# Optimization experiments

Hardware: AMD Instinct MI355X
Metric: run time of the kernel (lower is better)

Reference implementation:

```python
import jax, jax.numpy as jnp
import numpy as np

# Irreps spec: 256x0e + 128x1o + 64x2e + 32x3o (irreps_out == irreps_in)
MULS = (256, 128, 64, 32)          # multiplicities per irrep block
IRDIMS = (1, 3, 5, 7)              # 2l+1 per irrep block
FEAT_DIM = sum(m * d for m, d in zip(MULS, IRDIMS))   # 1184
W_DIM = sum(m * m for m in MULS)                       # 87040
BATCH = 131072


def setup_inputs() -> dict:
    key = jax.random.key(0)
    kx, kw = jax.random.split(key)
    x = jax.random.normal(kx, (BATCH, FEAT_DIM), dtype=jnp.float32)
    w = jax.random.normal(kw, (W_DIM,), dtype=jnp.float32)
    return {"x": x, "w": w}


def reference(x, w):
    """Equivariant linear: per-irrep block-diagonal matmul with 1/sqrt(mul_in) norm.

    x: [B, FEAT_DIM] in mul_ir layout (segments of [mul, 2l+1] flattened).
    w: [W_DIM] flat weights, segments of [mul_out, mul_in] flattened.
    """
    B = x.shape[0]
    outs = []
    xo = 0  # feature offset (static)
    wo = 0  # weight offset (static)
    for mul, d in zip(MULS, IRDIMS):
        seg = x[:, xo:xo + mul * d].reshape(B, mul, d)          # [B, u, i]
        wb = w[wo:wo + mul * mul].reshape(mul, mul)             # [v, u]
        c = 1.0 / np.sqrt(mul)                                  # path normalization
        y = jnp.einsum('vu,bui->bvi', wb * c, seg,
                       precision=jax.lax.Precision.HIGH)        # [B, v, i]
        outs.append(y.reshape(B, mul * d))
        xo += mul * d
        wo += mul * mul
    return jnp.concatenate(outs, axis=-1)  # [B, FEAT_DIM]
```

## Files before the change

kernel.cpp:

```cpp
#include <hip/hip_runtime.h>


typedef __attribute__((ext_vector_type(8))) __bf16 bf16x8;
typedef __attribute__((ext_vector_type(4))) float f32x4;

constexpr int FEAT = 1184;

template<int MUL, int D, int XO, int WO, int WAVES_M, int WAVES_N, int NT>
__global__ __launch_bounds__(256, 2)
void eqlin(const float* __restrict__ x, const float* __restrict__ w,
           float* __restrict__ out, int n_tiles, float cnorm)
{
    constexpr int KS   = MUL / 32;
    constexpr int ROWS = WAVES_M * 16;

    const int tid  = threadIdx.x;
    const int lane = tid & 63;
    const int wid  = tid >> 6;
    const int wm   = wid % WAVES_M;
    const int wn   = wid / WAVES_M;
    const int l16  = lane & 15;
    const int quad = lane >> 4;
    const int lk8  = quad * 8;

    bf16x8 bfrag[NT][KS];
#pragma unroll
    for (int nt = 0; nt < NT; ++nt) {
        const int v = (wn * NT + nt) * 16 + l16;
        const float* wp = w + WO + (long)v * MUL;
#pragma unroll
        for (int ks = 0; ks < KS; ++ks) {
            const int u0 = ks * 32 + lk8;
#pragma unroll
            for (int j = 0; j < 8; ++j)
                bfrag[nt][ks][j] = (__bf16)(wp[u0 + j] * cnorm);
        }
    }

    for (int t = blockIdx.x; t < n_tiles; t += gridDim.x) {
        if (WAVES_N > 1) __syncthreads();

        const int mbase = t * ROWS + wm * 16;

        bf16x8 afrag[KS];
        {
            const int m = mbase + l16;
            if (D == 1) {
                const float* xp = x + (long)m * FEAT + XO;
#pragma unroll
                for (int ks = 0; ks < KS; ++ks) {
                    const float4 p0 = *(const float4*)(xp + ks * 32 + lk8);
                    const float4 p1 = *(const float4*)(xp + ks * 32 + lk8 + 4);
                    afrag[ks][0] = (__bf16)p0.x; afrag[ks][1] = (__bf16)p0.y;
                    afrag[ks][2] = (__bf16)p0.z; afrag[ks][3] = (__bf16)p0.w;
                    afrag[ks][4] = (__bf16)p1.x; afrag[ks][5] = (__bf16)p1.y;
                    afrag[ks][6] = (__bf16)p1.z; afrag[ks][7] = (__bf16)p1.w;
                }
            } else {
                const int b = m / D;
                const int i = m - b * D;
                const float* xp = x + (long)b * FEAT + XO + i;
#pragma unroll
                for (int ks = 0; ks < KS; ++ks) {
#pragma unroll
                    for (int j = 0; j < 8; ++j)
                        afrag[ks][j] = (__bf16)xp[(ks * 32 + lk8 + j) * D];
                }
            }
        }

        f32x4 acc[NT];
#pragma unroll
        for (int nt = 0; nt < NT; ++nt) acc[nt] = f32x4{0.f, 0.f, 0.f, 0.f};
#pragma unroll
        for (int ks = 0; ks < KS; ++ks)
#pragma unroll
            for (int nt = 0; nt < NT; ++nt)
                acc[nt] = __builtin_amdgcn_mfma_f32_16x16x32_bf16(
                    afrag[ks], bfrag[nt][ks], acc[nt], 0, 0, 0);

#pragma unroll
        for (int nt = 0; nt < NT; ++nt) {
            const int v = (wn * NT + nt) * 16 + l16;
#pragma unroll
            for (int r = 0; r < 4; ++r) {
                const int mm = mbase + quad * 4 + r;
                const int b = mm / D;
                const int i = mm - b * D;
                out[(long)b * FEAT + XO + v * D + i] = acc[nt][r];
            }
        }
    }
}

extern "C" void kernel_launch(void* const* d_in, const int* in_sizes, int n_in,
                              void* d_out, int out_size, void* d_ws, size_t ws_size,
                              hipStream_t stream) {
    const float* x = (const float*)d_in[0];
    const float* w = (const float*)d_in[1];
    float* out = (float*)d_out;

    eqlin<256, 1, 0, 0, 1, 4, 4>
        <<<dim3(512), dim3(256), 0, stream>>>(x, w, out, 8192, 0.0625f);
    eqlin<128, 3, 256, 65536, 2, 2, 4>
        <<<dim3(1024), dim3(256), 0, stream>>>(x, w, out, 12288, 0.088388347648318447f);
    eqlin<64, 5, 640, 81920, 4, 1, 4>
        <<<dim3(2048), dim3(256), 0, stream>>>(x, w, out, 10240, 0.125f);
    eqlin<32, 7, 960, 86016, 4, 1, 2>
        <<<dim3(2048), dim3(256), 0, stream>>>(x, w, out, 14336, 0.17677669529663689f);
}
```

Measured before the change: 1.247 ms.

## Stage x tiles through LDS with coalesced loads and double-buffered prefetch

Each block now loads a contiguous tile of batch rows with coalesced float4 reads and converts them to bf16. For d>1 it transposes them into a padded shared-memory buffer, so the old strided per-element gathers go away. A register prefetch of the next tile overlaps the global loads with the MFMA work, and waves are remapped across v-tiles and m-tiles. Output stores for D==1 are reoriented, and tile sizes, grid sizes and occupancy hints are retuned. In exchange the kernel uses more LDS, takes an extra barrier per tile, and may hit bank conflicts on the scalar transposed LDS writes.

Result: faster. 1.135 ms (-9.0%).

```diff
diff --git a/kernel.cpp b/kernel.cpp
--- a/kernel.cpp
+++ b/kernel.cpp
@@ -2,94 +2,168 @@
 
 
 typedef __attribute__((ext_vector_type(8))) __bf16 bf16x8;
+typedef __attribute__((ext_vector_type(4))) __bf16 bf16x4;
 typedef __attribute__((ext_vector_type(4))) float f32x4;
 
 constexpr int FEAT = 1184;
 
-template<int MUL, int D, int XO, int WO, int WAVES_M, int WAVES_N, int NT>
-__global__ __launch_bounds__(256, 2)
+template<int MUL, int D, int XO, int WO, int BT, int MINW>
+__global__ __launch_bounds__(256, MINW)
 void eqlin(const float* __restrict__ x, const float* __restrict__ w,
            float* __restrict__ out, int n_tiles, float cnorm)
 {
     constexpr int KS   = MUL / 32;
-    constexpr int ROWS = WAVES_M * 16;
+    constexpr int SEG  = MUL * D;
+    constexpr int VT   = MUL / 16;
+    constexpr int VTW  = (VT >= 4) ? VT / 4 : 1;
+    constexpr int MT   = BT * D / 16;
+    constexpr int MSP  = (VT >= 4) ? 1 : 4 / VT;
+    constexpr int MTW  = MT / MSP;
+    constexpr int Kp   = MUL + 8;
+    constexpr int BUFE = BT * D * Kp;
+    constexpr int NLD  = BT * SEG / 1024;
+
+    __shared__ __align__(16) __bf16 smem[2 * BUFE];
 
     const int tid  = threadIdx.x;
     const int lane = tid & 63;
     const int wid  = tid >> 6;
-    const int wm   = wid % WAVES_M;
-    const int wn   = wid / WAVES_M;
     const int l16  = lane & 15;
     const int quad = lane >> 4;
-    const int lk8  = quad * 8;
 
-    bf16x8 bfrag[NT][KS];
+    const int vt0 = (VT >= 4) ? wid * VTW : (wid & (VT - 1));
+    const int mt0 = (VT >= 4) ? 0 : (wid / VT) * MTW;
+
+    bf16x8 wfrag[VTW][KS];
 #pragma unroll
-    for (int nt = 0; nt < NT; ++nt) {
-        const int v = (wn * NT + nt) * 16 + l16;
-        const float* wp = w + WO + (long)v * MUL;
+    for (int vt = 0; vt < VTW; ++vt) {
+        const float* wp = w + WO + (long)((vt0 + vt) * 16 + l16) * MUL;
 #pragma unroll
         for (int ks = 0; ks < KS; ++ks) {
-            const int u0 = ks * 32 + lk8;
-#pragma unroll
-            for (int j = 0; j < 8; ++j)
-                bfrag[nt][ks][j] = (__bf16)(wp[u0 + j] * cnorm);
+            const float4 q0 = *(const float4*)(wp + ks * 32 + quad * 8);
+            const float4 q1 = *(const float4*)(wp + ks * 32 + quad * 8 + 4);
+            wfrag[vt][ks][0] = (__bf16)(q0.x * cnorm);
+            wfrag[vt][ks][1] = (__bf16)(q0.y * cnorm);
+            wfrag[vt][ks][2] = (__bf16)(q0.z * cnorm);
+            wfrag[vt][ks][3] = (__bf16)(q0.w * cnorm);
+            wfrag[vt][ks][4] = (__bf16)(q1.x * cnorm);
+            wfrag[vt][ks][5] = (__bf16)(q1.y * cnorm);
+            wfrag[vt][ks][6] = (__bf16)(q1.z * cnorm);
+            wfrag[vt][ks][7] = (__bf16)(q1.w * cnorm);
         }
     }
 
-    for (int t = blockIdx.x; t < n_tiles; t += gridDim.x) {
-        if (WAVES_N > 1) __syncthreads();
+    int xoff[NLD];
+#pragma unroll
+    for (int c = 0; c < NLD; ++c) {
+        const int e  = (c * 256 + tid) * 4;
+        const int bl = e / SEG;
+        xoff[c] = bl * FEAT + XO + (e - bl * SEG);
+    }
 
-        const int mbase = t * ROWS + wm * 16;
+    float4 pf[NLD];
 
-        bf16x8 afrag[KS];
-        {
-            const int m = mbase + l16;
-            if (D == 1) {
-                const float* xp = x + (long)m * FEAT + XO;
+    auto stage_load = [&](int tt) {
+        const float* xb = x + (long)tt * BT * FEAT;
 #pragma unroll
-                for (int ks = 0; ks < KS; ++ks) {
-                    const float4 p0 = *(const float4*)(xp + ks * 32 + lk8);
-                    const float4 p1 = *(const float4*)(xp + ks * 32 + lk8 + 4);
-                    afrag[ks][0] = (__bf16)p0.x; afrag[ks][1] = (__bf16)p0.y;
-                    afrag[ks][2] = (__bf16)p0.z; afrag[ks][3] = (__bf16)p0.w;
-                    afrag[ks][4] = (__bf16)p1.x; afrag[ks][5] = (__bf16)p1.y;
-                    afrag[ks][6] = (__bf16)p1.z; afrag[ks][7] = (__bf16)p1.w;
-                }
+        for (int c = 0; c < NLD; ++c)
+            pf[c] = *(const float4*)(xb + xoff[c]);
+    };
+
+    auto stage_write = [&](int hb) {
+        __bf16* dst = smem + hb * BUFE;
+#pragma unroll
+        for (int c = 0; c < NLD; ++c) {
+            const int e  = (c * 256 + tid) * 4;
+            const int bl = e / SEG;
+            const int fo = e - bl * SEG;
+            if constexpr (D == 1) {
+                bf16x4 v4;
+                v4[0] = (__bf16)pf[c].x; v4[1] = (__bf16)pf[c].y;
+                v4[2] = (__bf16)pf[c].z; v4[3] = (__bf16)pf[c].w;
+                *(bf16x4*)(dst + bl * Kp + fo) = v4;
             } else {
-                const int b = m / D;
-                const int i = m - b * D;
-                const float* xp = x + (long)b * FEAT + XO + i;
+                const float fv[4] = {pf[c].x, pf[c].y, pf[c].z, pf[c].w};
 #pragma unroll
-                for (int ks = 0; ks < KS; ++ks) {
-#pragma unroll
-                    for (int j = 0; j < 8; ++j)
-                        afrag[ks][j] = (__bf16)xp[(ks * 32 + lk8 + j) * D];
+                for (int j = 0; j < 4; ++j) {
+                    const int f = fo + j;
+                    const int u = f / D;
+                    const int i = f - u * D;
+                    dst[(bl * D + i) * Kp + u] = (__bf16)fv[j];
                 }
             }
         }
+    };
 
-        f32x4 acc[NT];
+    const int G = gridDim.x;
+    int t = blockIdx.x;
+
+    if (t < n_tiles) { stage_load(t); stage_write(0); }
+    __syncthreads();
+
+    int buf = 0;
+    for (; t < n_tiles; t += G) {
+        const int tn = t + G;
+        if (tn < n_tiles) stage_load(tn);
+
+        const __bf16* src = smem + buf * BUFE;
+        f32x4 acc[VTW][MTW];
 #pragma unroll
-        for (int nt = 0; nt < NT; ++nt) acc[nt] = f32x4{0.f, 0.f, 0.f, 0.f};
+        for (int vt = 0; vt < VTW; ++vt)
 #pragma unroll
-        for (int ks = 0; ks < KS; ++ks)
-#pragma unroll
-            for (int nt = 0; nt < NT; ++nt)
-                acc[nt] = __builtin_amdgcn_mfma_f32_16x16x32_bf16(
-                    afrag[ks], bfrag[nt][ks], acc[nt], 0, 0, 0);
+            for (int mt = 0; mt < MTW; ++mt)
+                acc[vt][mt] = f32x4{0.f, 0.f, 0.f, 0.f};
 
 #pragma unroll
-        for (int nt = 0; nt < NT; ++nt) {
-            const int v = (wn * NT + nt) * 16 + l16;
+        for (int mt = 0; mt < MTW; ++mt) {
+            const int m = (mt0 + mt) * 16 + l16;
+            bf16x8 xf[KS];
 #pragma unroll
-            for (int r = 0; r < 4; ++r) {
-                const int mm = mbase + quad * 4 + r;
-                const int b = mm / D;
-                const int i = mm - b * D;
-                out[(long)b * FEAT + XO + v * D + i] = acc[nt][r];
-            }
+            for (int ks = 0; ks < KS; ++ks)
+                xf[ks] = *(const bf16x8*)(src + m * Kp + ks * 32 + quad * 8);
+#pragma unroll
+            for (int ks = 0; ks < KS; ++ks)
+#pragma unroll
+                for (int vt = 0; vt < VTW; ++vt) {
+                    if constexpr (D == 1)
+                        acc[vt][mt] = __builtin_amdgcn_mfma_f32_16x16x32_bf16(
+                            xf[ks], wfrag[vt][ks], acc[vt][mt], 0, 0, 0);
+                    else
+                        acc[vt][mt] = __builtin_amdgcn_mfma_f32_16x16x32_bf16(
+                            wfrag[vt][ks], xf[ks], acc[vt][mt], 0, 0, 0);
+                }
         }
+
+        {
+            const long rb = (long)t * BT;
+#pragma unroll
+            for (int vt = 0; vt < VTW; ++vt)
+#pragma unroll
+                for (int mt = 0; mt < MTW; ++mt) {
+                    if constexpr (D == 1) {
+                        const int v = (vt0 + vt) * 16 + l16;
+#pragma unroll
+                        for (int r = 0; r < 4; ++r) {
+                            const long b = rb + (mt0 + mt) * 16 + quad * 4 + r;
+                            out[b * FEAT + XO + v] = acc[vt][mt][r];
+                        }
+                    } else {
+                        const int m  = (mt0 + mt) * 16 + l16;
+                        const int bl = m / D;
+                        const int i  = m - bl * D;
+#pragma unroll
+                        for (int r = 0; r < 4; ++r) {
+                            const int v = (vt0 + vt) * 16 + quad * 4 + r;
+                            out[(rb + bl) * FEAT + XO + v * D + i] =
+                                acc[vt][mt][r];
+                        }
+                    }
+                }
+        }
+
+        if (tn < n_tiles) stage_write(buf ^ 1);
+        __syncthreads();
+        buf ^= 1;
     }
 }
 
@@ -100,12 +174,12 @@
     const float* w = (const float*)d_in[1];
     float* out = (float*)d_out;
 
-    eqlin<256, 1, 0, 0, 1, 4, 4>
+    eqlin<256, 1,   0,     0, 16, 2>
         <<<dim3(512), dim3(256), 0, stream>>>(x, w, out, 8192, 0.0625f);
-    eqlin<128, 3, 256, 65536, 2, 2, 4>
-        <<<dim3(1024), dim3(256), 0, stream>>>(x, w, out, 12288, 0.088388347648318447f);
-    eqlin<64, 5, 640, 81920, 4, 1, 4>
-        <<<dim3(2048), dim3(256), 0, stream>>>(x, w, out, 10240, 0.125f);
-    eqlin<32, 7, 960, 86016, 4, 1, 2>
-        <<<dim3(2048), dim3(256), 0, stream>>>(x, w, out, 14336, 0.17677669529663689f);
+    eqlin<128, 3, 256, 65536, 16, 3>
+        <<<dim3(768), dim3(256), 0, stream>>>(x, w, out, 8192, 0.088388347648318447f);
+    eqlin< 64, 5, 640, 81920, 32, 3>
+        <<<dim3(768), dim3(256), 0, stream>>>(x, w, out, 4096, 0.125f);
+    eqlin< 32, 7, 960, 86016, 32, 4>
+        <<<dim3(1024), dim3(256), 0, stream>>>(x, w, out, 4096, 0.17677669529663689f);
 }
```
